# Kernel optimization log

Measured on AMD Instinct MI355X. Metric: run time of the kernel, lower is better.

The kernel has to match this reference:

```python
import jax, jax.numpy as jnp
import numpy as np

S, B, E2 = 128, 32, 1024   # src_len, batch, 2*encoder_hidden
DH = 512                   # decoder_hidden
AH = 32                    # attn_hidden
EMB = 256                  # embedding_dim
V = 32000                  # output_dim (vocab)


def setup_inputs() -> dict:
    key = jax.random.key(0)
    ks = jax.random.split(key, 14)
    sc = 0.02
    inp = {
        "encoder_output": jax.random.normal(ks[0], (S, B, E2), jnp.float32),
        "max_length": 48,
        "sos_token": 1,
        "emb": jax.random.normal(ks[1], (V, EMB), jnp.float32) * sc,
        "W1": jax.random.normal(ks[2], (AH, DH + E2), jnp.float32) * sc,
        "b1": jnp.zeros((AH,), jnp.float32),
        "W2": jax.random.normal(ks[3], (1, AH), jnp.float32) * sc,
        "b2": jnp.zeros((1,), jnp.float32),
        "W_ih": jax.random.normal(ks[4], (3 * DH, E2 + EMB), jnp.float32) * sc,
        "b_ih": jnp.zeros((3 * DH,), jnp.float32),
        "W_hh": jax.random.normal(ks[5], (3 * DH, DH), jnp.float32) * sc,
        "b_hh": jnp.zeros((3 * DH,), jnp.float32),
        "Wo": jax.random.normal(ks[6], (V, DH), jnp.float32) * sc,
        "bo": jnp.zeros((V,), jnp.float32),
    }
    return inp


def reference(encoder_output, max_length, sos_token, emb, W1, b1, W2, b2,
              W_ih, b_ih, W_hh, b_hh, Wo, bo):
    s, b, _ = encoder_output.shape
    dh = W_hh.shape[1]

    def step(carry, _):
        h, x_emb = carry                       # h: [B,DH], x_emb: [B,EMB]
        # Bahdanau-style attention: concat(hidden, enc) -> MLP -> softmax over S
        ai = jnp.concatenate(
            [jnp.broadcast_to(h[None], (s, b, dh)), encoder_output], axis=2)
        scores = jnp.maximum(ai @ W1.T + b1, 0.0) @ W2.T + b2   # [S,B,1]
        attn = jax.nn.softmax(scores[..., 0], axis=0)           # [S,B]
        context = jnp.einsum('sbe,sb->be', encoder_output, attn)  # [B,2E]
        # single-step GRU cell (torch gate order: r, z, n)
        x = jnp.concatenate([context, x_emb], axis=1)
        gi = x @ W_ih.T + b_ih
        gh = h @ W_hh.T + b_hh
        r = jax.nn.sigmoid(gi[:, :dh] + gh[:, :dh])
        z = jax.nn.sigmoid(gi[:, dh:2 * dh] + gh[:, dh:2 * dh])
        n = jnp.tanh(gi[:, 2 * dh:] + r * gh[:, 2 * dh:])
        h_new = (1.0 - z) * n + z * h
        logits = h_new @ Wo.T + bo                              # [B,V]
        ids = jnp.argmax(logits, axis=1)
        return (h_new, emb[ids]), logits

    h0 = jnp.zeros((b, dh), encoder_output.dtype)
    x0 = jnp.broadcast_to(emb[sos_token][None], (b, emb.shape[1]))
    _, out = jax.lax.scan(step, (h0, x0), None, length=max_length)
    return out  # [max_length, B, V]
```

## Files before the change

kernel.cpp:

```cpp
#include <hip/hip_runtime.h>
#include <hip/hip_bf16.h>
#include <math.h>

typedef __bf16 bf16x8 __attribute__((ext_vector_type(8)));
typedef __bf16 bf16x4 __attribute__((ext_vector_type(4)));
typedef float f32x4 __attribute__((ext_vector_type(4)));

#define S_LEN 128
#define BATCH 32
#define E2C 1024
#define DH 512
#define AH 32
#define EMBD 256
#define VOC 32000
#define TMAX 48
#define LCHN 250
#define CTXB 64

#define MFMA16(a, b, c) __builtin_amdgcn_mfma_f32_16x16x32_bf16((a), (b), (c), 0, 0, 0)

#define OFF_HF0   0
#define OFF_HH0   65536
#define OFF_HL0   98304
#define OFF_HF1   131072
#define OFF_HH1   196608
#define OFF_HL1   229376
#define OFF_XH    262144
#define OFF_XL    344064
#define OFF_ENCW1 425984
#define OFF_PVAL  950272
#define OFF_PIDX  983040
#define OFF_WOH   1015808
#define OFF_WOL   33783808
#define OFF_WIHH  66551808
#define OFF_WIHL  70483968
#define OFF_WHHH  74416128
#define OFF_WHHL  75988992
#define WS_REQ    77561856ULL

__device__ __forceinline__ void split8(const float* __restrict__ p,
                                       bf16x8& hi, bf16x8& lo) {
  const f32x4 v0 = *(const f32x4*)p;
  const f32x4 v1 = *(const f32x4*)(p + 4);
  float t[8] = {v0[0], v0[1], v0[2], v0[3], v1[0], v1[1], v1[2], v1[3]};
  #pragma unroll
  for (int i = 0; i < 8; i++) {
    const __bf16 h = (__bf16)t[i];
    hi[i] = h;
    lo[i] = (__bf16)(t[i] - (float)h);
  }
}

__global__ __launch_bounds__(256) void k_init(unsigned int* __restrict__ p) {
  p[blockIdx.x * 256 + threadIdx.x] = 0u;
}

__global__ __launch_bounds__(256) void k_encw1(const float* __restrict__ enc,
                                               const float* __restrict__ W1,
                                               float* __restrict__ encW1) {
  __shared__ float el[E2C];
  __shared__ float red[256];
  const int tid = threadIdx.x;
  const int blk = blockIdx.x;
  for (int i = 0; i < 4; i++)
    el[tid + i * 256] = enc[(size_t)blk * E2C + tid + i * 256];
  __syncthreads();
  const int j = tid >> 3, c = tid & 7;
  const float* wrow = W1 + (size_t)j * (DH + E2C) + DH;
  float p = 0.f;
  for (int k = c * 128; k < c * 128 + 128; k++) p += el[k] * wrow[k];
  red[tid] = p;
  __syncthreads();
  if (c < 4) red[tid] += red[tid + 4];
  __syncthreads();
  if (c < 2) red[tid] += red[tid + 2];
  __syncthreads();
  if (c == 0) encW1[(size_t)blk * AH + j] = red[tid] + red[tid + 1];
}

__global__ __launch_bounds__(256) void k_split4(const float* __restrict__ src,
                                                __bf16* __restrict__ dh,
                                                __bf16* __restrict__ dl, int n4) {
  const int i = blockIdx.x * 256 + threadIdx.x;
  if (i >= n4) return;
  const f32x4 v = ((const f32x4*)src)[i];
  bf16x4 h4, l4;
  #pragma unroll
  for (int j = 0; j < 4; j++) {
    const float x = v[j];
    const __bf16 h = (__bf16)x;
    h4[j] = h;
    l4[j] = (__bf16)(x - (float)h);
  }
  *(bf16x4*)(dh + (size_t)i * 4) = h4;
  *(bf16x4*)(dl + (size_t)i * 4) = l4;
}

__device__ __forceinline__ void ctx_block(int bc, int tid,
    const float* __restrict__ enc,
    const float* __restrict__ W1, const float* __restrict__ b1,
    const float* __restrict__ W2, const float* __restrict__ b2,
    const float* __restrict__ encW1, const float* __restrict__ hf,
    __bf16* __restrict__ xh, __bf16* __restrict__ xl,
    float* hs, float* hw, float* sc, float* red) {
  const int b = bc >> 1;
  const int part = bc & 1;

  if (tid < 256) {
    hs[tid] = hf[b * DH + tid];
    hs[tid + 256] = hf[b * DH + tid + 256];
  }
  __syncthreads();
  if (tid < 256) {
    const int j = tid >> 3, c = tid & 7;
    const float* wrow = W1 + (size_t)j * (DH + E2C);
    float p = 0.f;
    for (int k = c * 64; k < c * 64 + 64; k++) p += hs[k] * wrow[k];
    red[tid] = p;
  }
  __syncthreads();
  if (tid < 256 && (tid & 7) < 4) red[tid] += red[tid + 4];
  __syncthreads();
  if (tid < 256 && (tid & 7) < 2) red[tid] += red[tid + 2];
  __syncthreads();
  if (tid < 256 && (tid & 7) == 0) hw[tid >> 3] = red[tid] + red[tid + 1] + b1[tid >> 3];
  __syncthreads();

  float ex = 0.f;
  if (tid < S_LEN) {
    const float* ew = encW1 + ((size_t)tid * BATCH + b) * AH;
    float sum = b2[0];
    #pragma unroll
    for (int j = 0; j < AH; j++) {
      const float v = ew[j] + hw[j];
      sum += fmaxf(v, 0.f) * W2[j];
    }
    sc[tid] = sum;
  }
  __syncthreads();
  if (tid < 128) red[tid] = sc[tid];
  __syncthreads();
  for (int off = 64; off >= 1; off >>= 1) {
    if (tid < off) red[tid] = fmaxf(red[tid], red[tid + off]);
    __syncthreads();
  }
  const float mx = red[0];
  __syncthreads();
  if (tid < 128) { ex = expf(sc[tid] - mx); red[tid] = ex; }
  __syncthreads();
  for (int off = 64; off >= 1; off >>= 1) {
    if (tid < off) red[tid] += red[tid + off];
    __syncthreads();
  }
  const float ssum = red[0];
  if (tid < 128) sc[tid] = ex / ssum;
  __syncthreads();

  const int e0 = part * 512 + tid;
  float aa = 0.f;
  for (int s = 0; s < S_LEN; s++)
    aa += sc[s] * enc[((size_t)s * BATCH + b) * E2C + e0];
  const __bf16 ch = (__bf16)aa;
  xh[b * 1024 + e0] = ch;
  xl[b * 1024 + e0] = (__bf16)(aa - (float)ch);
}

__global__ __launch_bounds__(512) void k_ctx0(
    const float* __restrict__ enc,
    const float* __restrict__ W1, const float* __restrict__ b1,
    const float* __restrict__ W2, const float* __restrict__ b2,
    const float* __restrict__ encW1, const float* __restrict__ hf,
    __bf16* __restrict__ xh, __bf16* __restrict__ xl) {
  __shared__ float hs[DH];
  __shared__ float hw[AH];
  __shared__ float sc[S_LEN];
  __shared__ float red[256];
  ctx_block(blockIdx.x, threadIdx.x, enc, W1, b1, W2, b2, encW1, hf, xh, xl,
            hs, hw, sc, red);
}

template<bool PRE>
__global__ __launch_bounds__(256) void k_gru(int t,
    const int* __restrict__ sos, const float* __restrict__ emb,
    const float* __restrict__ pval, const int* __restrict__ pidx,
    const __bf16* __restrict__ xh, const __bf16* __restrict__ xl,
    const float* __restrict__ Wih, const float* __restrict__ bih,
    const float* __restrict__ Whh, const float* __restrict__ bhh,
    const __bf16* __restrict__ Wihh, const __bf16* __restrict__ Wihl,
    const __bf16* __restrict__ Whhh, const __bf16* __restrict__ Whhl,
    const float* __restrict__ hf_in, const __bf16* __restrict__ hh_in,
    const __bf16* __restrict__ hl_in,
    float* __restrict__ hf_out, __bf16* __restrict__ hh_out,
    __bf16* __restrict__ hl_out) {
  __shared__ float lds[4][8][256];
  __shared__ int ids[32];
  const int tid = threadIdx.x;

  if (t == 0) {
    if (tid < 32) {
      int id = sos[0];
      if (id < 0 || id >= VOC) id = 0;
      ids[tid] = id;
    }
  } else {
    float* sv = &lds[0][0][0];
    int*   si = (int*)&lds[1][0][0];
    const int b = tid >> 3, c0 = tid & 7;
    float bv = -INFINITY; int bi = 0x7fffffff;
    for (int c = c0; c < LCHN; c += 8) {
      const float v = pval[b * 256 + c]; const int ix = pidx[b * 256 + c];
      if (v > bv || (v == bv && ix < bi)) { bv = v; bi = ix; }
    }
    sv[tid] = bv; si[tid] = bi;
    __syncthreads();
    for (int off = 4; off >= 1; off >>= 1) {
      if (c0 < off) {
        const float ov = sv[tid + off]; const int oi = si[tid + off];
        if (ov > sv[tid] || (ov == sv[tid] && oi < si[tid])) { sv[tid] = ov; si[tid] = oi; }
      }
      __syncthreads();
    }
    if (c0 == 0) {
      int id = si[tid];
      if (id < 0 || id >= VOC) id = 0;
      ids[b] = id;
    }
  }
  __syncthreads();

  const int wv = tid >> 6;
  const int lane = tid & 63;
  const int q = lane >> 4;
  const int ln = lane & 15;
  const int d = blockIdx.x * 16 + ln;
  const int id0 = ids[ln];
  const int id1 = ids[16 + ln];

  f32x4 acc[4][2];
  const f32x4 z4 = {0.f, 0.f, 0.f, 0.f};
  #pragma unroll
  for (int tt = 0; tt < 4; tt++) { acc[tt][0] = z4; acc[tt][1] = z4; }

  #pragma unroll
  for (int i = 0; i < 14; i++) {
    const int ka = wv * 32 + i * 128 + q * 8;
    bf16x8 ah0, al0, ah1, al1;
    if (i < 8) {
      ah0 = *(const bf16x8*)(xh + ln * 1024 + ka);
      ah1 = *(const bf16x8*)(xh + (16 + ln) * 1024 + ka);
      al0 = *(const bf16x8*)(xl + ln * 1024 + ka);
      al1 = *(const bf16x8*)(xl + (16 + ln) * 1024 + ka);
    } else if (i < 10) {
      const int kb = ka - 1024;
      split8(emb + (size_t)id0 * EMBD + kb, ah0, al0);
      split8(emb + (size_t)id1 * EMBD + kb, ah1, al1);
    } else {
      const int kb = ka - 1280;
      ah0 = *(const bf16x8*)(hh_in + ln * 512 + kb);
      ah1 = *(const bf16x8*)(hh_in + (16 + ln) * 512 + kb);
      al0 = *(const bf16x8*)(hl_in + ln * 512 + kb);
      al1 = *(const bf16x8*)(hl_in + (16 + ln) * 512 + kb);
    }
    #pragma unroll
    for (int g = 0; g < 3; g++) {
      bf16x8 bh, bl;
      if (PRE) {
        if (i < 10) {
          bh = *(const bf16x8*)(Wihh + (size_t)(g * 512 + d) * 1280 + ka);
          bl = *(const bf16x8*)(Wihl + (size_t)(g * 512 + d) * 1280 + ka);
        } else {
          bh = *(const bf16x8*)(Whhh + (size_t)(g * 512 + d) * 512 + (ka - 1280));
          bl = *(const bf16x8*)(Whhl + (size_t)(g * 512 + d) * 512 + (ka - 1280));
        }
      } else {
        if (i < 10) split8(Wih + (size_t)(g * 512 + d) * 1280 + ka, bh, bl);
        else        split8(Whh + (size_t)(g * 512 + d) * 512 + (ka - 1280), bh, bl);
      }
      const int tt = (g < 2) ? g : ((i < 10) ? 2 : 3);
      acc[tt][0] = MFMA16(ah0, bh, acc[tt][0]);
      acc[tt][0] = MFMA16(al0, bh, acc[tt][0]);
      acc[tt][0] = MFMA16(ah0, bl, acc[tt][0]);
      acc[tt][1] = MFMA16(ah1, bh, acc[tt][1]);
      acc[tt][1] = MFMA16(al1, bh, acc[tt][1]);
      acc[tt][1] = MFMA16(ah1, bl, acc[tt][1]);
    }
  }

  #pragma unroll
  for (int tt = 0; tt < 4; tt++)
    #pragma unroll
    for (int mt = 0; mt < 2; mt++)
      #pragma unroll
      for (int r = 0; r < 4; r++)
        lds[wv][tt * 2 + mt][(q * 4 + r) * 16 + ln] = acc[tt][mt][r];
  __syncthreads();
  for (int idx = tid; idx < 8 * 256; idx += 256) {
    const int tt = idx >> 8, e = idx & 255;
    lds[0][tt][e] += lds[1][tt][e] + lds[2][tt][e] + lds[3][tt][e];
  }
  __syncthreads();

  for (int u = tid; u < 512; u += 256) {
    const int b = u >> 4, dd = u & 15;
    const int mt = b >> 4;
    const int e = (b & 15) * 16 + dd;
    const int dg = blockIdx.x * 16 + dd;
    const float rp  = lds[0][0 * 2 + mt][e] + bih[dg]        + bhh[dg];
    const float zp  = lds[0][1 * 2 + mt][e] + bih[DH + dg]   + bhh[DH + dg];
    const float gin = lds[0][2 * 2 + mt][e] + bih[2 * DH + dg];
    const float ghn = lds[0][3 * 2 + mt][e] + bhh[2 * DH + dg];
    const float rg = 1.f / (1.f + expf(-rp));
    const float zg = 1.f / (1.f + expf(-zp));
    const float ng = tanhf(gin + rg * ghn);
    const float hp = hf_in[b * DH + dg];
    const float hn = (1.f - zg) * ng + zg * hp;
    hf_out[b * DH + dg] = hn;
    const __bf16 hi = (__bf16)hn;
    hh_out[b * DH + dg] = hi;
    hl_out[b * DH + dg] = (__bf16)(hn - (float)hi);
  }
}

template<bool PRE>
__global__ __launch_bounds__(512) void k_logctx(
    const float* __restrict__ enc,
    const float* __restrict__ W1, const float* __restrict__ b1,
    const float* __restrict__ W2, const float* __restrict__ b2,
    const float* __restrict__ encW1,
    const float* __restrict__ Wo, const float* __restrict__ bo,
    const __bf16* __restrict__ Woh, const __bf16* __restrict__ Wol,
    const float* __restrict__ hf, const __bf16* __restrict__ hh,
    const __bf16* __restrict__ hl,
    float* __restrict__ outp, float* __restrict__ pval, int* __restrict__ pidx,
    __bf16* __restrict__ xh, __bf16* __restrict__ xl) {
  __shared__ union {
    struct { float hs[DH]; float hw[AH]; float sc[S_LEN]; float red[256]; } c;
    struct { float lv[256]; int li[256]; } l;
  } sm;
  const int tid = threadIdx.x;
  const int blk = blockIdx.x;

  if (blk >= LCHN) {
    ctx_block(blk - LCHN, tid, enc, W1, b1, W2, b2, encW1, hf, xh, xl,
              sm.c.hs, sm.c.hw, sm.c.sc, sm.c.red);
    return;
  }

  const int w = tid >> 6;
  const int lane = tid & 63;
  const int quad = lane >> 4;
  const int ln = lane & 15;
  const int v0 = blk * 128;
  const int vr = v0 + w * 16 + ln;

  f32x4 acc[2];
  const f32x4 z4 = {0.f, 0.f, 0.f, 0.f};
  acc[0] = z4; acc[1] = z4;

  const __bf16* wrh = Woh + (size_t)vr * 512;
  const __bf16* wrl = Wol + (size_t)vr * 512;
  const float*  wrf = Wo  + (size_t)vr * 512;

  #pragma unroll 2
  for (int kk = 0; kk < 512; kk += 32) {
    const int ka = kk + quad * 8;
    const bf16x8 fh0 = *(const bf16x8*)(hh + ln * 512 + ka);
    const bf16x8 fh1 = *(const bf16x8*)(hh + (16 + ln) * 512 + ka);
    const bf16x8 fl0 = *(const bf16x8*)(hl + ln * 512 + ka);
    const bf16x8 fl1 = *(const bf16x8*)(hl + (16 + ln) * 512 + ka);
    bf16x8 bh, bl;
    if (PRE) {
      bh = *(const bf16x8*)(wrh + ka);
      bl = *(const bf16x8*)(wrl + ka);
    } else {
      split8(wrf + ka, bh, bl);
    }
    acc[0] = MFMA16(fh0, bh, acc[0]);
    acc[0] = MFMA16(fl0, bh, acc[0]);
    acc[0] = MFMA16(fh0, bl, acc[0]);
    acc[1] = MFMA16(fh1, bh, acc[1]);
    acc[1] = MFMA16(fl1, bh, acc[1]);
    acc[1] = MFMA16(fh1, bl, acc[1]);
  }

  float bv[2][4]; int bi[2][4];
  const float bias = bo[vr];
  #pragma unroll
  for (int mt = 0; mt < 2; mt++) {
    #pragma unroll
    for (int r = 0; r < 4; r++) {
      const float val = acc[mt][r] + bias;
      const int b = mt * 16 + quad * 4 + r;
      __builtin_nontemporal_store(val, &outp[(size_t)b * VOC + vr]);
      bv[mt][r] = val; bi[mt][r] = vr;
    }
  }
  #pragma unroll
  for (int m = 1; m < 16; m <<= 1) {
    #pragma unroll
    for (int mt = 0; mt < 2; mt++) {
      #pragma unroll
      for (int r = 0; r < 4; r++) {
        const float ov = __shfl_xor(bv[mt][r], m, 64);
        const int oi = __shfl_xor(bi[mt][r], m, 64);
        if (ov > bv[mt][r] || (ov == bv[mt][r] && oi < bi[mt][r])) {
          bv[mt][r] = ov; bi[mt][r] = oi;
        }
      }
    }
  }
  if (ln == 0) {
    #pragma unroll
    for (int mt = 0; mt < 2; mt++)
      for (int r = 0; r < 4; r++) {
        const int b = mt * 16 + quad * 4 + r;
        sm.l.lv[w * 32 + b] = bv[mt][r];
        sm.l.li[w * 32 + b] = bi[mt][r];
      }
  }
  __syncthreads();
  if (tid < 32) {
    float bbv = sm.l.lv[tid]; int bbi = sm.l.li[tid];
    for (int w2 = 1; w2 < 8; w2++) {
      const float ov = sm.l.lv[w2 * 32 + tid]; const int oi = sm.l.li[w2 * 32 + tid];
      if (ov > bbv || (ov == bbv && oi < bbi)) { bbv = ov; bbi = oi; }
    }
    pval[tid * 256 + blk] = bbv;
    pidx[tid * 256 + blk] = bbi;
  }
}

extern "C" void kernel_launch(void* const* d_in, const int* in_sizes, int n_in,
                              void* d_out, int out_size, void* d_ws, size_t ws_size,
                              hipStream_t stream) {
  const float* enc = (const float*)d_in[0];
  const int* sos = (const int*)d_in[2];
  const float* emb = (const float*)d_in[3];
  const float* W1 = (const float*)d_in[4];
  const float* b1 = (const float*)d_in[5];
  const float* W2 = (const float*)d_in[6];
  const float* b2 = (const float*)d_in[7];
  const float* Wih = (const float*)d_in[8];
  const float* bih = (const float*)d_in[9];
  const float* Whh = (const float*)d_in[10];
  const float* bhh = (const float*)d_in[11];
  const float* Wo = (const float*)d_in[12];
  const float* bo = (const float*)d_in[13];

  char* ws = (char*)d_ws;
  float* hf[2]  = {(float*)(ws + OFF_HF0),  (float*)(ws + OFF_HF1)};
  __bf16* hh[2] = {(__bf16*)(ws + OFF_HH0), (__bf16*)(ws + OFF_HH1)};
  __bf16* hl[2] = {(__bf16*)(ws + OFF_HL0), (__bf16*)(ws + OFF_HL1)};
  __bf16* xh = (__bf16*)(ws + OFF_XH);
  __bf16* xl = (__bf16*)(ws + OFF_XL);
  float* encW1 = (float*)(ws + OFF_ENCW1);
  float* pval = (float*)(ws + OFF_PVAL);
  int* pidx = (int*)(ws + OFF_PIDX);
  __bf16* Woh  = (__bf16*)(ws + OFF_WOH);
  __bf16* Wol  = (__bf16*)(ws + OFF_WOL);
  __bf16* Wihh = (__bf16*)(ws + OFF_WIHH);
  __bf16* Wihl = (__bf16*)(ws + OFF_WIHL);
  __bf16* Whhh = (__bf16*)(ws + OFF_WHHH);
  __bf16* Whhl = (__bf16*)(ws + OFF_WHHL);

  k_init<<<128, 256, 0, stream>>>((unsigned int*)ws);
  k_encw1<<<S_LEN * BATCH, 256, 0, stream>>>(enc, W1, encW1);

  float* out = (float*)d_out;
  const bool pre = (ws_size >= WS_REQ);
  if (pre) {
    k_split4<<<16000, 256, 0, stream>>>(Wo,  Woh,  Wol,  4096000);
    k_split4<<<1920,  256, 0, stream>>>(Wih, Wihh, Wihl, 491520);
    k_split4<<<768,   256, 0, stream>>>(Whh, Whhh, Whhl, 196608);
  }
  k_ctx0<<<CTXB, 512, 0, stream>>>(enc, W1, b1, W2, b2, encW1, hf[0], xh, xl);

  for (int t = 0; t < TMAX; t++) {
    const int p = t & 1;
    if (pre) {
      k_gru<true><<<32, 256, 0, stream>>>(t, sos, emb, pval, pidx, xh, xl,
                                          Wih, bih, Whh, bhh,
                                          Wihh, Wihl, Whhh, Whhl,
                                          hf[p], hh[p], hl[p],
                                          hf[p ^ 1], hh[p ^ 1], hl[p ^ 1]);
      k_logctx<true><<<LCHN + CTXB, 512, 0, stream>>>(enc, W1, b1, W2, b2, encW1,
                                          Wo, bo, Woh, Wol,
                                          hf[p ^ 1], hh[p ^ 1], hl[p ^ 1],
                                          out + (size_t)t * BATCH * VOC,
                                          pval, pidx, xh, xl);
    } else {
      k_gru<false><<<32, 256, 0, stream>>>(t, sos, emb, pval, pidx, xh, xl,
                                          Wih, bih, Whh, bhh,
                                          Wihh, Wihl, Whhh, Whhl,
                                          hf[p], hh[p], hl[p],
                                          hf[p ^ 1], hh[p ^ 1], hl[p ^ 1]);
      k_logctx<false><<<LCHN + CTXB, 512, 0, stream>>>(enc, W1, b1, W2, b2, encW1,
                                          Wo, bo, Woh, Wol,
                                          hf[p ^ 1], hh[p ^ 1], hl[p ^ 1],
                                          out + (size_t)t * BATCH * VOC,
                                          pval, pidx, xh, xl);
    }
  }
}
```

Baseline: 3.341 ms.

## Halve block size in logits/context kernel, give each wave two vocab tiles

The fused logits+context kernel drops from 512 to 256 threads per block. Each wave in the logits part now computes two 16-column vocab tiles, so the hidden-state A fragments are reused across both tiles. The context blocks are split four ways per batch row instead of two, giving 128 ctx blocks, and they are now scheduled first in the grid. The goal is better A-fragment reuse and finer scheduling granularity, at the cost of more accumulator registers and duplicated attention-score work across four blocks per batch row.

```diff
diff --git a/kernel.cpp b/kernel.cpp
--- a/kernel.cpp
+++ b/kernel.cpp
@@ -15,7 +15,7 @@
 #define VOC 32000
 #define TMAX 48
 #define LCHN 250
-#define CTXB 64
+#define CTXB 128
 
 #define MFMA16(a, b, c) __builtin_amdgcn_mfma_f32_16x16x32_bf16((a), (b), (c), 0, 0, 0)
 
@@ -103,15 +103,13 @@
     const float* __restrict__ encW1, const float* __restrict__ hf,
     __bf16* __restrict__ xh, __bf16* __restrict__ xl,
     float* hs, float* hw, float* sc, float* red) {
-  const int b = bc >> 1;
-  const int part = bc & 1;
-
-  if (tid < 256) {
-    hs[tid] = hf[b * DH + tid];
-    hs[tid + 256] = hf[b * DH + tid + 256];
-  }
-  __syncthreads();
-  if (tid < 256) {
+  const int b = bc >> 2;
+  const int part = bc & 3;
+
+  hs[tid] = hf[b * DH + tid];
+  hs[tid + 256] = hf[b * DH + tid + 256];
+  __syncthreads();
+  {
     const int j = tid >> 3, c = tid & 7;
     const float* wrow = W1 + (size_t)j * (DH + E2C);
     float p = 0.f;
@@ -119,11 +117,11 @@
     red[tid] = p;
   }
   __syncthreads();
-  if (tid < 256 && (tid & 7) < 4) red[tid] += red[tid + 4];
-  __syncthreads();
-  if (tid < 256 && (tid & 7) < 2) red[tid] += red[tid + 2];
-  __syncthreads();
-  if (tid < 256 && (tid & 7) == 0) hw[tid >> 3] = red[tid] + red[tid + 1] + b1[tid >> 3];
+  if ((tid & 7) < 4) red[tid] += red[tid + 4];
+  __syncthreads();
+  if ((tid & 7) < 2) red[tid] += red[tid + 2];
+  __syncthreads();
+  if ((tid & 7) == 0) hw[tid >> 3] = red[tid] + red[tid + 1] + b1[tid >> 3];
   __syncthreads();
 
   float ex = 0.f;
@@ -156,7 +154,7 @@
   if (tid < 128) sc[tid] = ex / ssum;
   __syncthreads();
 
-  const int e0 = part * 512 + tid;
+  const int e0 = part * 256 + tid;
   float aa = 0.f;
   for (int s = 0; s < S_LEN; s++)
     aa += sc[s] * enc[((size_t)s * BATCH + b) * E2C + e0];
@@ -165,7 +163,7 @@
   xl[b * 1024 + e0] = (__bf16)(aa - (float)ch);
 }
 
-__global__ __launch_bounds__(512) void k_ctx0(
+__global__ __launch_bounds__(256) void k_ctx0(
     const float* __restrict__ enc,
     const float* __restrict__ W1, const float* __restrict__ b1,
     const float* __restrict__ W2, const float* __restrict__ b2,
@@ -322,7 +320,7 @@
 }
 
 template<bool PRE>
-__global__ __launch_bounds__(512) void k_logctx(
+__global__ __launch_bounds__(256) void k_logctx(
     const float* __restrict__ enc,
     const float* __restrict__ W1, const float* __restrict__ b1,
     const float* __restrict__ W2, const float* __restrict__ b2,
@@ -335,31 +333,29 @@
     __bf16* __restrict__ xh, __bf16* __restrict__ xl) {
   __shared__ union {
     struct { float hs[DH]; float hw[AH]; float sc[S_LEN]; float red[256]; } c;
-    struct { float lv[256]; int li[256]; } l;
+    struct { float lv[128]; int li[128]; } l;
   } sm;
   const int tid = threadIdx.x;
-  const int blk = blockIdx.x;
-
-  if (blk >= LCHN) {
-    ctx_block(blk - LCHN, tid, enc, W1, b1, W2, b2, encW1, hf, xh, xl,
+
+  if (blockIdx.x < CTXB) {
+    ctx_block(blockIdx.x, tid, enc, W1, b1, W2, b2, encW1, hf, xh, xl,
               sm.c.hs, sm.c.hw, sm.c.sc, sm.c.red);
     return;
   }
+  const int chunk = blockIdx.x - CTXB;
 
   const int w = tid >> 6;
   const int lane = tid & 63;
   const int quad = lane >> 4;
   const int ln = lane & 15;
-  const int v0 = blk * 128;
-  const int vr = v0 + w * 16 + ln;
-
-  f32x4 acc[2];
+  const int v0 = chunk * 128;
+
+  f32x4 acc[2][2];
   const f32x4 z4 = {0.f, 0.f, 0.f, 0.f};
-  acc[0] = z4; acc[1] = z4;
-
-  const __bf16* wrh = Woh + (size_t)vr * 512;
-  const __bf16* wrl = Wol + (size_t)vr * 512;
-  const float*  wrf = Wo  + (size_t)vr * 512;
+  #pragma unroll
+  for (int m = 0; m < 2; m++)
+    #pragma unroll
+    for (int n = 0; n < 2; n++) acc[m][n] = z4;
 
   #pragma unroll 2
   for (int kk = 0; kk < 512; kk += 32) {
@@ -368,31 +364,44 @@
     const bf16x8 fh1 = *(const bf16x8*)(hh + (16 + ln) * 512 + ka);
     const bf16x8 fl0 = *(const bf16x8*)(hl + ln * 512 + ka);
     const bf16x8 fl1 = *(const bf16x8*)(hl + (16 + ln) * 512 + ka);
-    bf16x8 bh, bl;
-    if (PRE) {
-      bh = *(const bf16x8*)(wrh + ka);
-      bl = *(const bf16x8*)(wrl + ka);
-    } else {
-      split8(wrf + ka, bh, bl);
-    }
-    acc[0] = MFMA16(fh0, bh, acc[0]);
-    acc[0] = MFMA16(fl0, bh, acc[0]);
-    acc[0] = MFMA16(fh0, bl, acc[0]);
-    acc[1] = MFMA16(fh1, bh, acc[1]);
-    acc[1] = MFMA16(fl1, bh, acc[1]);
-    acc[1] = MFMA16(fh1, bl, acc[1]);
+    #pragma unroll
+    for (int nt = 0; nt < 2; nt++) {
+      const int vr = v0 + (w * 2 + nt) * 16 + ln;
+      bf16x8 bh, bl;
+      if (PRE) {
+        bh = *(const bf16x8*)(Woh + (size_t)vr * 512 + ka);
+        bl = *(const bf16x8*)(Wol + (size_t)vr * 512 + ka);
+      } else {
+        split8(Wo + (size_t)vr * 512 + ka, bh, bl);
+      }
+      acc[0][nt] = MFMA16(fh0, bh, acc[0][nt]);
+      acc[0][nt] = MFMA16(fl0, bh, acc[0][nt]);
+      acc[0][nt] = MFMA16(fh0, bl, acc[0][nt]);
+      acc[1][nt] = MFMA16(fh1, bh, acc[1][nt]);
+      acc[1][nt] = MFMA16(fl1, bh, acc[1][nt]);
+      acc[1][nt] = MFMA16(fh1, bl, acc[1][nt]);
+    }
   }
 
   float bv[2][4]; int bi[2][4];
-  const float bias = bo[vr];
-  #pragma unroll
-  for (int mt = 0; mt < 2; mt++) {
-    #pragma unroll
-    for (int r = 0; r < 4; r++) {
-      const float val = acc[mt][r] + bias;
-      const int b = mt * 16 + quad * 4 + r;
-      __builtin_nontemporal_store(val, &outp[(size_t)b * VOC + vr]);
-      bv[mt][r] = val; bi[mt][r] = vr;
+  #pragma unroll
+  for (int m = 0; m < 2; m++)
+    #pragma unroll
+    for (int r = 0; r < 4; r++) { bv[m][r] = -INFINITY; bi[m][r] = 0x7fffffff; }
+
+  #pragma unroll
+  for (int nt = 0; nt < 2; nt++) {
+    const int v = v0 + (w * 2 + nt) * 16 + ln;
+    const float bias = bo[v];
+    #pragma unroll
+    for (int mt = 0; mt < 2; mt++) {
+      #pragma unroll
+      for (int r = 0; r < 4; r++) {
+        const float val = acc[mt][nt][r] + bias;
+        const int b = mt * 16 + quad * 4 + r;
+        __builtin_nontemporal_store(val, &outp[(size_t)b * VOC + v]);
+        if (val > bv[mt][r]) { bv[mt][r] = val; bi[mt][r] = v; }
+      }
     }
   }
   #pragma unroll
@@ -421,12 +430,12 @@
   __syncthreads();
   if (tid < 32) {
     float bbv = sm.l.lv[tid]; int bbi = sm.l.li[tid];
-    for (int w2 = 1; w2 < 8; w2++) {
+    for (int w2 = 1; w2 < 4; w2++) {
       const float ov = sm.l.lv[w2 * 32 + tid]; const int oi = sm.l.li[w2 * 32 + tid];
       if (ov > bbv || (ov == bbv && oi < bbi)) { bbv = ov; bbi = oi; }
     }
-    pval[tid * 256 + blk] = bbv;
-    pidx[tid * 256 + blk] = bbi;
+    pval[tid * 256 + chunk] = bbv;
+    pidx[tid * 256 + chunk] = bbi;
   }
 }
 
@@ -473,7 +482,7 @@
     k_split4<<<1920,  256, 0, stream>>>(Wih, Wihh, Wihl, 491520);
     k_split4<<<768,   256, 0, stream>>>(Whh, Whhh, Whhl, 196608);
   }
-  k_ctx0<<<CTXB, 512, 0, stream>>>(enc, W1, b1, W2, b2, encW1, hf[0], xh, xl);
+  k_ctx0<<<CTXB, 256, 0, stream>>>(enc, W1, b1, W2, b2, encW1, hf[0], xh, xl);
 
   for (int t = 0; t < TMAX; t++) {
     const int p = t & 1;
@@ -483,7 +492,7 @@
                                           Wihh, Wihl, Whhh, Whhl,
                                           hf[p], hh[p], hl[p],
                                           hf[p ^ 1], hh[p ^ 1], hl[p ^ 1]);
-      k_logctx<true><<<LCHN + CTXB, 512, 0, stream>>>(enc, W1, b1, W2, b2, encW1,
+      k_logctx<true><<<CTXB + LCHN, 256, 0, stream>>>(enc, W1, b1, W2, b2, encW1,
                                           Wo, bo, Woh, Wol,
                                           hf[p ^ 1], hh[p ^ 1], hl[p ^ 1],
                                           out + (size_t)t * BATCH * VOC,
@@ -494,7 +503,7 @@
                                           Wihh, Wihl, Whhh, Whhl,
                                           hf[p], hh[p], hl[p],
                                           hf[p ^ 1], hh[p ^ 1], hl[p ^ 1]);
-      k_logctx<false><<<LCHN + CTXB, 512, 0, stream>>>(enc, W1, b1, W2, b2, encW1,
+      k_logctx<false><<<CTXB + LCHN, 256, 0, stream>>>(enc, W1, b1, W2, b2, encW1,
                                           Wo, bo, Woh, Wol,
                                           hf[p ^ 1], hh[p ^ 1], hl[p ^ 1],
                                           out + (size_t)t * BATCH * VOC,
```

Result: faster. 2.965 ms (-11.3%).
